# Optimization experiments

Hardware: AMD Instinct MI355X
Metric: run time of the kernel (lower is better)

Reference implementation:

```python
import jax, jax.numpy as jnp
import numpy as np

B, N, M = 4, 8192, 8192


def setup_inputs() -> dict:
    key = jax.random.key(0)
    k1, k2, k3, k4 = jax.random.split(key, 4)
    xyz1 = jax.random.normal(k1, (B, N, 3), dtype=jnp.float32)
    xyz2 = jax.random.normal(k2, (B, M, 3), dtype=jnp.float32)
    weights1 = jax.random.uniform(k3, (B, N), dtype=jnp.float32)
    weights2 = jax.random.uniform(k4, (B, M), dtype=jnp.float32)
    return {"xyz1": xyz1, "xyz2": xyz2, "weights1": weights1, "weights2": weights2}


def _chamfer_dists(xyz1, xyz2):
    # Squared L2 pairwise distances via the ||a||^2 + ||b||^2 - 2 a.b identity
    # (avoids materializing a [B, N, M, 3] difference tensor).
    sq1 = jnp.sum(xyz1 * xyz1, axis=-1)            # [B, N]
    sq2 = jnp.sum(xyz2 * xyz2, axis=-1)            # [B, M]
    dots = jnp.einsum("bnc,bmc->bnm", xyz1, xyz2)  # [B, N, M]
    d = sq1[:, :, None] + sq2[:, None, :] - 2.0 * dots
    d = jnp.maximum(d, 0.0)
    dist1 = jnp.min(d, axis=2)  # [B, N] nearest in xyz2 for each point in xyz1
    dist2 = jnp.min(d, axis=1)  # [B, M] nearest in xyz1 for each point in xyz2
    return dist1, dist2


def reference(xyz1, xyz2, weights1, weights2):
    dist1, dist2 = _chamfer_dists(xyz1, xyz2)
    dist1 = dist1 * weights1
    dist2 = dist2 * weights2
    dist1_avg = jnp.sum(dist1) / jnp.sum(weights1)
    dist2_avg = jnp.sum(dist2) / jnp.sum(weights2)
    return (dist1_avg + dist2_avg) / 2.0
```

## Files before the change

kernel.cpp:

```cpp
#include <hip/hip_runtime.h>

#define TPB 256
constexpr int Bsz  = 4;
constexpr int Npts = 8192;
constexpr int Mpts = 8192;
constexpr int PTS  = Bsz * Npts;
constexpr int Q    = 8;
constexpr int QPB  = TPB * Q;
constexpr int CPS  = 128;
constexpr int S    = Mpts / CPS;
constexpr int CP   = CPS / 2;
constexpr int RBLK = 64;

typedef float f32x2 __attribute__((ext_vector_type(2)));

__device__ __forceinline__ f32x2 sp2(float v)             { f32x2 r; r.x = v; r.y = v; return r; }
__device__ __forceinline__ f32x2 min2(f32x2 a, f32x2 b)   { return __builtin_elementwise_min(a, b); }
__device__ __forceinline__ f32x2 fma2(f32x2 a, f32x2 b, f32x2 c) { return __builtin_elementwise_fma(a, b, c); }

__global__ void __launch_bounds__(TPB, 4) chamfer_fused_kernel(
    const float* __restrict__ xyz1, const float* __restrict__ xyz2,
    unsigned int* __restrict__ partials)
{
    const int chunksPerBatch = Npts / QPB;
    int bid   = blockIdx.x;
    int s     = bid % S;
    int chunk = (bid / S) % chunksPerBatch;
    int batch = bid / (S * chunksPerBatch);

    __shared__ float cnx[CPS], cny[CPS], cnz[CPS], cw[CPS];
    __shared__ unsigned int colb[CPS];
    int c0 = batch * Mpts + s * CPS;
    if (threadIdx.x < CPS) {
        int ci = c0 + threadIdx.x;
        float x = xyz2[ci * 3 + 0];
        float y = xyz2[ci * 3 + 1];
        float z = xyz2[ci * 3 + 2];
        cnx[threadIdx.x] = -2.f * x;
        cny[threadIdx.x] = -2.f * y;
        cnz[threadIdx.x] = -2.f * z;
        cw [threadIdx.x] = x * x + y * y + z * z;
        colb[threadIdx.x] = 0x7f7fffffu;
    }

    int qbase = batch * Npts + chunk * QPB + threadIdx.x;
    float qx[Q], qy[Q], qz[Q], q2[Q], rowbest[Q];
#pragma unroll
    for (int k = 0; k < Q; ++k) {
        int q = qbase + k * TPB;
        qx[k] = xyz1[q * 3 + 0];
        qy[k] = xyz1[q * 3 + 1];
        qz[k] = xyz1[q * 3 + 2];
        q2[k] = fmaf(qx[k], qx[k], fmaf(qy[k], qy[k], qz[k] * qz[k]));
        rowbest[k] = 3.4e38f;
    }
    __syncthreads();

    const f32x2* cnx2 = (const f32x2*)cnx;
    const f32x2* cny2 = (const f32x2*)cny;
    const f32x2* cnz2 = (const f32x2*)cnz;
    const f32x2* cw2  = (const f32x2*)cw;
    const int skew = threadIdx.x & 63;

#pragma unroll 4
    for (int j0 = 0; j0 < CP; ++j0) {
        int p = (j0 + skew) & (CP - 1);
        f32x2 cx = cnx2[p];
        f32x2 cy = cny2[p];
        f32x2 cz = cnz2[p];
        f32x2 cw2v = cw2[p];
        f32x2 cmin = sp2(3.4e38f);
#pragma unroll
        for (int k = 0; k < Q; ++k) {
            f32x2 acc = cw2v + q2[k];
            acc = fma2(cz, sp2(qz[k]), acc);
            acc = fma2(cy, sp2(qy[k]), acc);
            acc = fma2(cx, sp2(qx[k]), acc);
            rowbest[k] = fminf(rowbest[k], fminf(acc.x, acc.y));
            cmin = min2(cmin, acc);
        }
        atomicMin(&colb[2 * p + 0], __float_as_uint(fmaxf(cmin.x, 0.f)));
        atomicMin(&colb[2 * p + 1], __float_as_uint(fmaxf(cmin.y, 0.f)));
    }

#pragma unroll
    for (int k = 0; k < Q; ++k) {
        int q = qbase + k * TPB;
        atomicMin(&partials[q], __float_as_uint(fmaxf(rowbest[k], 0.f)));
    }

    __syncthreads();
    if (threadIdx.x < CPS)
        atomicMin(&partials[PTS + c0 + threadIdx.x], colb[threadIdx.x]);
}

__global__ void __launch_bounds__(TPB) reduce_kernel(
    const float* __restrict__ partials,
    const float* __restrict__ w1, const float* __restrict__ w2,
    float2* __restrict__ slots)
{
    int gid = blockIdx.x * TPB + threadIdx.x;
    int dir = gid >> 13;
    int idx = gid & 8191;
    const float4* d4 = (const float4*)(partials + (size_t)dir * PTS);
    const float4* w4 = (const float4*)(dir ? w2 : w1);
    float4 d = d4[idx], w = w4[idx];
    float c = d.x * w.x + d.y * w.y + d.z * w.z + d.w * w.w;
    float s = w.x + w.y + w.z + w.w;

    for (int off = 32; off; off >>= 1) {
        c += __shfl_down(c, off);
        s += __shfl_down(s, off);
    }
    __shared__ float sc[4], ss[4];
    int lane = threadIdx.x & 63, wid = threadIdx.x >> 6;
    if (lane == 0) { sc[wid] = c; ss[wid] = s; }
    __syncthreads();
    if (threadIdx.x == 0) {
        slots[blockIdx.x] =
            make_float2(sc[0] + sc[1] + sc[2] + sc[3],
                        ss[0] + ss[1] + ss[2] + ss[3]);
    }
}

__global__ void __launch_bounds__(64) final_kernel(
    const float2* __restrict__ slots, float* __restrict__ out)
{
    float2 v = slots[threadIdx.x];
    for (int off = 16; off; off >>= 1) {
        v.x += __shfl_down(v.x, off, 32);
        v.y += __shfl_down(v.y, off, 32);
    }
    float c1 = __shfl(v.x, 32), s1 = __shfl(v.y, 32);
    if (threadIdx.x == 0)
        out[0] = 0.5f * (v.x / v.y + c1 / s1);
}

extern "C" void kernel_launch(void* const* d_in, const int* in_sizes, int n_in,
                              void* d_out, int out_size, void* d_ws, size_t ws_size,
                              hipStream_t stream) {
    const float* xyz1 = (const float*)d_in[0];
    const float* xyz2 = (const float*)d_in[1];
    const float* w1   = (const float*)d_in[2];
    const float* w2   = (const float*)d_in[3];
    float* out = (float*)d_out;

    unsigned int* partials = (unsigned int*)d_ws;
    float2* slots = (float2*)((char*)d_ws + (size_t)2 * PTS * sizeof(unsigned int));

    int nblocks = Bsz * (Npts / QPB) * S;
    chamfer_fused_kernel<<<nblocks, TPB, 0, stream>>>(xyz1, xyz2, partials);
    reduce_kernel<<<RBLK, TPB, 0, stream>>>((const float*)partials, w1, w2, slots);
    final_kernel<<<1, 64, 0, stream>>>(slots, out);
}
```

Baseline: 93.57 us.

## Compute pairwise distances with bf16x3-split MFMA instead of FP32 VALU

Adds a prep kernel that splits each coordinate and squared norm into three bf16 parts and packs them into MFMA fragment layouts. Each distance tile is then one 16x16x32 bf16 MFMA with FP32 accumulation, and row and column minima are reduced with shuffles and atomics. This moves the O(NM) distance work off the vector ALU onto the matrix cores. It adds an extra kernel launch and workspace traffic, and the bf16 split may cost some accuracy.

```diff
diff --git a/kernel.cpp b/kernel.cpp
--- a/kernel.cpp
+++ b/kernel.cpp
@@ -5,93 +5,152 @@
 constexpr int Npts = 8192;
 constexpr int Mpts = 8192;
 constexpr int PTS  = Bsz * Npts;
-constexpr int Q    = 8;
-constexpr int QPB  = TPB * Q;
-constexpr int CPS  = 128;
-constexpr int S    = Mpts / CPS;
-constexpr int CP   = CPS / 2;
+constexpr int QT_PER_B = Npts / 16;
+constexpr int CT_PER_B = Mpts / 16;
 constexpr int RBLK = 64;
 
-typedef float f32x2 __attribute__((ext_vector_type(2)));
-
-__device__ __forceinline__ f32x2 sp2(float v)             { f32x2 r; r.x = v; r.y = v; return r; }
-__device__ __forceinline__ f32x2 min2(f32x2 a, f32x2 b)   { return __builtin_elementwise_min(a, b); }
-__device__ __forceinline__ f32x2 fma2(f32x2 a, f32x2 b, f32x2 c) { return __builtin_elementwise_fma(a, b, c); }
-
-__global__ void __launch_bounds__(TPB, 4) chamfer_fused_kernel(
+typedef __attribute__((ext_vector_type(8))) short short8;
+typedef __attribute__((ext_vector_type(4))) float f32x4;
+
+__device__ __forceinline__ unsigned short bfh(float v) {
+    unsigned u = __float_as_uint(v);
+    return (unsigned short)((u + 0x7fffu + ((u >> 16) & 1u)) >> 16);
+}
+__device__ __forceinline__ float b2f(unsigned short h) {
+    return __uint_as_float(((unsigned)h) << 16);
+}
+__device__ __forceinline__ void split3(float v, unsigned short& h,
+                                       unsigned short& m, unsigned short& l) {
+    h = bfh(v); float fh = b2f(h);
+    m = bfh(v - fh); float fm = b2f(m);
+    l = bfh(v - fh - fm);
+}
+
+__device__ __forceinline__ unsigned short pickA(int o, unsigned short h,
+                                                unsigned short m, unsigned short l) {
+    return o < 3 ? h : (o < 5 ? m : l);
+}
+__device__ __forceinline__ unsigned short pickB(int o, unsigned short h,
+                                                unsigned short m, unsigned short l) {
+    return (o == 1 || o == 4) ? m : (o == 2 ? l : h);
+}
+
+__global__ void __launch_bounds__(TPB) prep_kernel(
     const float* __restrict__ xyz1, const float* __restrict__ xyz2,
+    short* __restrict__ aQ, short* __restrict__ bC)
+{
+    int id   = blockIdx.x * TPB + threadIdx.x;
+    int side = id >> 17;
+    int tl   = id & 131071;
+    int tile = tl >> 6, lane = tl & 63;
+    int r = lane & 15, g = lane >> 4;
+
+    const float* src = side ? xyz2 : xyz1;
+    int p = tile * 16 + r;
+    float x = src[p * 3 + 0], y = src[p * 3 + 1], z = src[p * 3 + 2];
+    float n = fmaf(x, x, fmaf(y, y, z * z));
+    float s = side ? 1.f : -2.f;
+
+    unsigned short xh, xm, xl, yh, ym, yl, zh, zm, zl, nh, nm, nl;
+    split3(s * x, xh, xm, xl);
+    split3(s * y, yh, ym, yl);
+    split3(s * z, zh, zm, zl);
+    split3(n, nh, nm, nl);
+    const unsigned short ONE = 0x3F80;
+
+    short8 v;
+#pragma unroll
+    for (int j = 0; j < 8; ++j) {
+        int k = g * 8 + j;
+        unsigned short u = 0;
+        if (k < 18) {
+            int c = k / 6, o = k - 6 * c;
+            unsigned short h = c == 0 ? xh : (c == 1 ? yh : zh);
+            unsigned short m = c == 0 ? xm : (c == 1 ? ym : zm);
+            unsigned short l = c == 0 ? xl : (c == 1 ? yl : zl);
+            u = side ? pickB(o, h, m, l) : pickA(o, h, m, l);
+        } else if (k < 21) {
+            u = side ? ONE : (k == 18 ? nh : (k == 19 ? nm : nl));
+        } else if (k < 24) {
+            u = side ? (k == 21 ? nh : (k == 22 ? nm : nl)) : ONE;
+        }
+        v[j] = (short)u;
+    }
+    short8* dst = (short8*)(side ? bC : aQ);
+    dst[tile * 64 + lane] = v;
+}
+
+__global__ void __launch_bounds__(TPB, 4) chamfer_mfma_kernel(
+    const short* __restrict__ aQ, const short* __restrict__ bC,
     unsigned int* __restrict__ partials)
 {
-    const int chunksPerBatch = Npts / QPB;
-    int bid   = blockIdx.x;
-    int s     = bid % S;
-    int chunk = (bid / S) % chunksPerBatch;
-    int batch = bid / (S * chunksPerBatch);
-
-    __shared__ float cnx[CPS], cny[CPS], cnz[CPS], cw[CPS];
-    __shared__ unsigned int colb[CPS];
-    int c0 = batch * Mpts + s * CPS;
-    if (threadIdx.x < CPS) {
-        int ci = c0 + threadIdx.x;
-        float x = xyz2[ci * 3 + 0];
-        float y = xyz2[ci * 3 + 1];
-        float z = xyz2[ci * 3 + 2];
-        cnx[threadIdx.x] = -2.f * x;
-        cny[threadIdx.x] = -2.f * y;
-        cnz[threadIdx.x] = -2.f * z;
-        cw [threadIdx.x] = x * x + y * y + z * z;
-        colb[threadIdx.x] = 0x7f7fffffu;
-    }
-
-    int qbase = batch * Npts + chunk * QPB + threadIdx.x;
-    float qx[Q], qy[Q], qz[Q], q2[Q], rowbest[Q];
-#pragma unroll
-    for (int k = 0; k < Q; ++k) {
-        int q = qbase + k * TPB;
-        qx[k] = xyz1[q * 3 + 0];
-        qy[k] = xyz1[q * 3 + 1];
-        qz[k] = xyz1[q * 3 + 2];
-        q2[k] = fmaf(qx[k], qx[k], fmaf(qy[k], qy[k], qz[k] * qz[k]));
-        rowbest[k] = 3.4e38f;
-    }
+    int bid = blockIdx.x;
+    int linear = (bid & 7) * 128 + (bid >> 3);
+    int batch = linear >> 8;
+    int qs = (linear >> 4) & 15;
+    int cs = linear & 15;
+    int w = threadIdx.x >> 6, lane = threadIdx.x & 63;
+
+    int qtile0 = batch * QT_PER_B + qs * 32 + w * 8;
+    int ctile0 = batch * CT_PER_B + cs * 32;
+
+    const short8* aT = (const short8*)aQ;
+    const short8* bT = (const short8*)bC;
+
+    __shared__ unsigned int colb[512];
+    colb[threadIdx.x]       = 0x7f7fffffu;
+    colb[threadIdx.x + 256] = 0x7f7fffffu;
+
+    short8 afrag[8];
+#pragma unroll
+    for (int t = 0; t < 8; ++t) afrag[t] = aT[(qtile0 + t) * 64 + lane];
+
+    const f32x4 inf4 = {3.4e38f, 3.4e38f, 3.4e38f, 3.4e38f};
+    const f32x4 zero4 = {0.f, 0.f, 0.f, 0.f};
+    f32x4 rowp[8];
+#pragma unroll
+    for (int t = 0; t < 8; ++t) rowp[t] = inf4;
     __syncthreads();
 
-    const f32x2* cnx2 = (const f32x2*)cnx;
-    const f32x2* cny2 = (const f32x2*)cny;
-    const f32x2* cnz2 = (const f32x2*)cnz;
-    const f32x2* cw2  = (const f32x2*)cw;
-    const int skew = threadIdx.x & 63;
-
-#pragma unroll 4
-    for (int j0 = 0; j0 < CP; ++j0) {
-        int p = (j0 + skew) & (CP - 1);
-        f32x2 cx = cnx2[p];
-        f32x2 cy = cny2[p];
-        f32x2 cz = cnz2[p];
-        f32x2 cw2v = cw2[p];
-        f32x2 cmin = sp2(3.4e38f);
-#pragma unroll
-        for (int k = 0; k < Q; ++k) {
-            f32x2 acc = cw2v + q2[k];
-            acc = fma2(cz, sp2(qz[k]), acc);
-            acc = fma2(cy, sp2(qy[k]), acc);
-            acc = fma2(cx, sp2(qx[k]), acc);
-            rowbest[k] = fminf(rowbest[k], fminf(acc.x, acc.y));
-            cmin = min2(cmin, acc);
+    for (int ct = 0; ct < 32; ++ct) {
+        short8 bfrag = bT[(ctile0 + ct) * 64 + lane];
+        f32x4 d[8];
+#pragma unroll
+        for (int t = 0; t < 8; ++t)
+            d[t] = __builtin_amdgcn_mfma_f32_16x16x32_bf16(afrag[t], bfrag, zero4, 0, 0, 0);
+
+        float cmin = 3.4e38f;
+#pragma unroll
+        for (int t = 0; t < 8; ++t) {
+            rowp[t] = __builtin_elementwise_min(rowp[t], d[t]);
+            cmin = fminf(cmin, fminf(fminf(d[t][0], d[t][1]), fminf(d[t][2], d[t][3])));
         }
-        atomicMin(&colb[2 * p + 0], __float_as_uint(fmaxf(cmin.x, 0.f)));
-        atomicMin(&colb[2 * p + 1], __float_as_uint(fmaxf(cmin.y, 0.f)));
-    }
-
-#pragma unroll
-    for (int k = 0; k < Q; ++k) {
-        int q = qbase + k * TPB;
-        atomicMin(&partials[q], __float_as_uint(fmaxf(rowbest[k], 0.f)));
+        cmin = fminf(cmin, __shfl_xor(cmin, 16));
+        cmin = fminf(cmin, __shfl_xor(cmin, 32));
+        if (lane < 16)
+            atomicMin(&colb[ct * 16 + lane], __float_as_uint(fmaxf(cmin, 0.f)));
+    }
+
+#pragma unroll
+    for (int t = 0; t < 8; ++t) {
+#pragma unroll
+        for (int i = 0; i < 4; ++i) {
+            float v = rowp[t][i];
+            v = fminf(v, __shfl_xor(v, 1));
+            v = fminf(v, __shfl_xor(v, 2));
+            v = fminf(v, __shfl_xor(v, 4));
+            v = fminf(v, __shfl_xor(v, 8));
+            if ((lane & 15) == 0) {
+                int q = (qtile0 + t) * 16 + (lane >> 4) * 4 + i;
+                atomicMin(&partials[q], __float_as_uint(fmaxf(v, 0.f)));
+            }
+        }
     }
 
     __syncthreads();
-    if (threadIdx.x < CPS)
-        atomicMin(&partials[PTS + c0 + threadIdx.x], colb[threadIdx.x]);
+    int cbase = PTS + ctile0 * 16;
+    atomicMin(&partials[cbase + threadIdx.x],       colb[threadIdx.x]);
+    atomicMin(&partials[cbase + threadIdx.x + 256], colb[threadIdx.x + 256]);
 }
 
 __global__ void __launch_bounds__(TPB) reduce_kernel(
@@ -147,9 +206,11 @@
 
     unsigned int* partials = (unsigned int*)d_ws;
     float2* slots = (float2*)((char*)d_ws + (size_t)2 * PTS * sizeof(unsigned int));
-
-    int nblocks = Bsz * (Npts / QPB) * S;
-    chamfer_fused_kernel<<<nblocks, TPB, 0, stream>>>(xyz1, xyz2, partials);
+    short* aQ = (short*)((char*)d_ws + (1u << 20));
+    short* bC = (short*)((char*)d_ws + (4u << 20));
+
+    prep_kernel<<<1024, TPB, 0, stream>>>(xyz1, xyz2, aQ, bC);
+    chamfer_mfma_kernel<<<1024, TPB, 0, stream>>>(aQ, bC, partials);
     reduce_kernel<<<RBLK, TPB, 0, stream>>>((const float*)partials, w1, w2, slots);
     final_kernel<<<1, 64, 0, stream>>>(slots, out);
 }
```

New measurement: 115.9 us. 1.24x slower.
